# Kernel tuning notes

Hardware: AMD Instinct MI355X
Metric: run time of the kernel (lower is better)

The kernel has to match this reference:

```python
import jax, jax.numpy as jnp
import numpy as np

TEMP = 0.05
EPS = 1e-8  # torch CosineSimilarity default eps


def _normalize(x):
    # torch cosine_similarity clamps norm at eps
    n = jnp.maximum(jnp.linalg.norm(x, axis=-1, keepdims=True), EPS)
    return x / n


def setup_inputs() -> dict:
    key = jax.random.key(0)
    k1, k2, k3 = jax.random.split(key, 3)
    N, D = 4096, 1024
    return {
        "repr_sent": jax.random.normal(k1, (N, D), dtype=jnp.float32),
        "repr_pos": jax.random.normal(k2, (N, D), dtype=jnp.float32),
        "repr_neg": jax.random.normal(k3, (N, D), dtype=jnp.float32),
    }


def reference(repr_sent, repr_pos, repr_neg):
    # Normalize then GEMM instead of broadcasting an [N, 2N, D] intermediate.
    s = _normalize(repr_sent)            # [N, D]
    p = _normalize(repr_pos)             # [N, D]
    n = _normalize(repr_neg)             # [N, D]
    cand = jnp.concatenate([p, n], axis=0)           # [2N, D]
    sim = jnp.einsum("nd,md->nm", s, cand) / TEMP    # [N, 2N]
    # Cross-entropy with labels = arange(N) (positive is the i-th column)
    logz = jax.nn.logsumexp(sim, axis=-1)            # [N]
    N_ = sim.shape[0]
    pos_logit = jnp.diagonal(sim[:, :N_])            # sim[i, i]
    loss = jnp.mean(logz - pos_logit)
    return loss
```

## Files before the change

kernel.cpp:

```cpp
#include <hip/hip_runtime.h>
#include <stdint.h>

#define N_ROWS 4096
#define D_DIM  1024
#define N_CAND 8192
#define TEMP_INV 20.0f
#define QSCALE 508.0f
#define OUT_SCALE (TEMP_INV / (QSCALE * QSCALE))

#define BM 256
#define BN 256
#define BK 64
#define NT 16

typedef __attribute__((ext_vector_type(4))) int   i32x4;

using gvoid = __attribute__((address_space(1))) void;
using lvoid = __attribute__((address_space(3))) void;

#define BAR() __builtin_amdgcn_s_barrier()
#define SCHED0() __builtin_amdgcn_sched_barrier(0)

__global__ __launch_bounds__(256) void prep_kernel(
    const float* __restrict__ s, const float* __restrict__ p,
    const float* __restrict__ ng, unsigned char* __restrict__ s_q,
    unsigned char* __restrict__ cand_q, float* __restrict__ rowsum) {
  const int row = blockIdx.x;
  const int t = threadIdx.x;
  const float* src;
  unsigned char* dst;
  if (row < N_ROWS) {
    src = s + (size_t)row * D_DIM;
    dst = s_q + (size_t)row * D_DIM;
  } else if (row < 2 * N_ROWS) {
    src = p + (size_t)(row - N_ROWS) * D_DIM;
    dst = cand_q + (size_t)(row - N_ROWS) * D_DIM;
  } else {
    src = ng + (size_t)(row - 2 * N_ROWS) * D_DIM;
    dst = cand_q + (size_t)(row - N_ROWS) * D_DIM;
  }

  float4 v = reinterpret_cast<const float4*>(src)[t];
  float ss = v.x * v.x + v.y * v.y + v.z * v.z + v.w * v.w;
#pragma unroll
  for (int m = 32; m >= 1; m >>= 1) ss += __shfl_xor(ss, m, 64);
  __shared__ float red[4];
  const int w = t >> 6, l = t & 63;
  if (l == 0) red[w] = ss;
  __syncthreads();
  const float tot = red[0] + red[1] + red[2] + red[3];
  const float qs = QSCALE / fmaxf(sqrtf(tot), 1e-8f);

  auto q8 = [&](float x) -> unsigned {
    return (unsigned)((int)rintf(fminf(fmaxf(x * qs, -127.0f), 127.0f))) &
           0xffu;
  };
  const unsigned pk =
      q8(v.x) | (q8(v.y) << 8) | (q8(v.z) << 16) | (q8(v.w) << 24);
  *reinterpret_cast<unsigned*>(dst + t * 4) = pk;

  if (t == 0 && row < N_ROWS) rowsum[row] = 0.0f;
}

__global__ __launch_bounds__(512) void gemm_lse_kernel(
    const unsigned char* __restrict__ s_q,
    const unsigned char* __restrict__ cand_q,
    float* __restrict__ rowsum, float* __restrict__ pos) {
  __shared__ __align__(16) unsigned char lds[4 * 32768];

  const int t = threadIdx.x;
  const int w = t >> 6;
  const int l = t & 63;
  const int g = l >> 4;
  const int rl = l & 15;
  const int wm = w >> 2;
  const int wn = w & 3;
  const int slot = (g + (rl >> 1)) & 3;
  const int rowBase = blockIdx.y * BM;
  const int colBase = blockIdx.x * BN;

  i32x4 acc[8][4] = {};
  i32x4 af[8];
  i32x4 bf[4];

  const int sRow = t >> 2;
  const int sSlotL = ((t & 3) - (t >> 3)) & 3;
  const unsigned char* gA =
      s_q + (size_t)(rowBase + sRow) * D_DIM + sSlotL * 16;
  const unsigned char* gB =
      cand_q + (size_t)(colBase + sRow) * D_DIM + sSlotL * 16;

  auto stage = [&](int T) {
    const int buf = (T & 3) * 32768;
    const size_t ko = (size_t)T * 64;
#pragma unroll
    for (int h = 0; h < 2; ++h) {
      __builtin_amdgcn_global_load_lds(
          (const gvoid*)(gA + ko + (size_t)h * (128 * D_DIM)),
          (lvoid*)(lds + buf + h * 8192 + t * 16), 16, 0, 0);
      __builtin_amdgcn_global_load_lds(
          (const gvoid*)(gB + ko + (size_t)h * (128 * D_DIM)),
          (lvoid*)(lds + buf + 16384 + h * 8192 + t * 16), 16, 0, 0);
    }
  };

  stage(0); stage(1);
  asm volatile("s_waitcnt vmcnt(4)" ::: "memory");
  SCHED0();
  BAR(); SCHED0();

  for (int T = 0; T < NT; ++T) {
    const unsigned char* A = lds + (T & 3) * 32768;
    const unsigned char* B = A + 16384;
#pragma unroll
    for (int m = 0; m < 8; ++m) {
      const int r = wm * 128 + m * 16 + rl;
      af[m] = *reinterpret_cast<const i32x4*>(A + r * 64 + slot * 16);
    }
#pragma unroll
    for (int n = 0; n < 4; ++n) {
      const int r = wn * 64 + n * 16 + rl;
      bf[n] = *reinterpret_cast<const i32x4*>(B + r * 64 + slot * 16);
    }
    if (T + 2 < NT) stage(T + 2);

    __builtin_amdgcn_s_setprio(1);
#pragma unroll
    for (int m = 0; m < 8; ++m)
#pragma unroll
      for (int n = 0; n < 4; ++n)
        acc[m][n] = __builtin_amdgcn_mfma_i32_16x16x64_i8(
            af[m], bf[n], acc[m][n], 0, 0, 0);
    __builtin_amdgcn_s_setprio(0);

    if (T <= NT - 3) {
      asm volatile("s_waitcnt vmcnt(4)" ::: "memory");
    } else if (T == NT - 2) {
      asm volatile("s_waitcnt vmcnt(0)" ::: "memory");
    }
    SCHED0();
    BAR(); SCHED0();
  }

  __syncthreads();
  float* red = reinterpret_cast<float*>(lds);
  if (t < BM) red[t] = 0.0f;
  __syncthreads();

#pragma unroll
  for (int m = 0; m < 8; ++m) {
#pragma unroll
    for (int j = 0; j < 4; ++j) {
      const int rloc = wm * 128 + m * 16 + g * 4 + j;
      const int rowg = rowBase + rloc;
      float sm = 0.0f;
#pragma unroll
      for (int n = 0; n < 4; ++n) {
        const int colg = colBase + wn * 64 + n * 16 + rl;
        const float simv = (float)acc[m][n][j] * OUT_SCALE;
        if (colg == rowg) pos[rowg] = simv;
        sm += __expf(simv - TEMP_INV);
      }
      sm += __shfl_xor(sm, 1, 64);
      sm += __shfl_xor(sm, 2, 64);
      sm += __shfl_xor(sm, 4, 64);
      sm += __shfl_xor(sm, 8, 64);
      if (rl == 0) atomicAdd(&red[rloc], sm);
    }
  }
  __syncthreads();
  if (t < BM) atomicAdd(&rowsum[rowBase + t], red[t]);
}

__global__ __launch_bounds__(1024) void loss_kernel(
    const float* __restrict__ rowsum, const float* __restrict__ pos,
    float* __restrict__ out) {
  const int t = threadIdx.x;
  float acc = 0.0f;
  for (int i = t; i < N_ROWS; i += 1024)
    acc += TEMP_INV + logf(rowsum[i]) - pos[i];
#pragma unroll
  for (int m = 32; m >= 1; m >>= 1) acc += __shfl_xor(acc, m, 64);
  __shared__ float red[16];
  const int w = t >> 6, l = t & 63;
  if (l == 0) red[w] = acc;
  __syncthreads();
  if (t == 0) {
    float tot = 0.0f;
#pragma unroll
    for (int i = 0; i < 16; ++i) tot += red[i];
    out[0] = tot / (float)N_ROWS;
  }
}

extern "C" void kernel_launch(void* const* d_in, const int* in_sizes, int n_in,
                              void* d_out, int out_size, void* d_ws,
                              size_t ws_size, hipStream_t stream) {
  (void)in_sizes; (void)n_in; (void)out_size; (void)ws_size;
  const float* s = (const float*)d_in[0];
  const float* p = (const float*)d_in[1];
  const float* ng = (const float*)d_in[2];

  unsigned char* s_q = (unsigned char*)d_ws;
  unsigned char* cand_q = s_q + (size_t)N_ROWS * D_DIM;
  float* rowsum = (float*)(cand_q + (size_t)N_CAND * D_DIM);
  float* pos = rowsum + N_ROWS;
  float* out = (float*)d_out;

  prep_kernel<<<dim3(3 * N_ROWS), dim3(256), 0, stream>>>(s, p, ng, s_q,
                                                          cand_q, rowsum);
  gemm_lse_kernel<<<dim3(N_CAND / BN, N_ROWS / BM), dim3(512), 0, stream>>>(
      s_q, cand_q, rowsum, pos);
  loss_kernel<<<dim3(1), dim3(1024), 0, stream>>>(rowsum, pos, out);
}
```

Before: 64.42 us.

## Load A fragments directly from global memory and stage only B through LDS

```diff
diff --git a/kernel.cpp b/kernel.cpp
--- a/kernel.cpp
+++ b/kernel.cpp
@@ -13,7 +13,7 @@
 #define BK 64
 #define NT 16
 
-typedef __attribute__((ext_vector_type(4))) int   i32x4;
+typedef __attribute__((ext_vector_type(4))) int i32x4;
 
 using gvoid = __attribute__((address_space(1))) void;
 using lvoid = __attribute__((address_space(3))) void;
@@ -66,76 +66,72 @@
     const unsigned char* __restrict__ s_q,
     const unsigned char* __restrict__ cand_q,
     float* __restrict__ rowsum, float* __restrict__ pos) {
-  __shared__ __align__(16) unsigned char lds[4 * 32768];
+  __shared__ __align__(16) unsigned char lds[4 * 16384];
 
   const int t = threadIdx.x;
   const int w = t >> 6;
   const int l = t & 63;
   const int g = l >> 4;
   const int rl = l & 15;
-  const int wm = w >> 2;
-  const int wn = w & 3;
+  const int wm = w >> 1;
+  const int wn = w & 1;
   const int slot = (g + (rl >> 1)) & 3;
   const int rowBase = blockIdx.y * BM;
   const int colBase = blockIdx.x * BN;
 
-  i32x4 acc[8][4] = {};
-  i32x4 af[8];
-  i32x4 bf[4];
+  i32x4 acc[4][8] = {};
+  i32x4 af[4];
+  i32x4 bf[8];
+
+  const unsigned char* gAf =
+      s_q + (size_t)(rowBase + wm * 64 + rl) * D_DIM + g * 16;
 
   const int sRow = t >> 2;
   const int sSlotL = ((t & 3) - (t >> 3)) & 3;
-  const unsigned char* gA =
-      s_q + (size_t)(rowBase + sRow) * D_DIM + sSlotL * 16;
   const unsigned char* gB =
       cand_q + (size_t)(colBase + sRow) * D_DIM + sSlotL * 16;
 
-  auto stage = [&](int T) {
-    const int buf = (T & 3) * 32768;
+  auto stageB = [&](int T) {
+    const int buf = (T & 3) * 16384;
     const size_t ko = (size_t)T * 64;
-#pragma unroll
-    for (int h = 0; h < 2; ++h) {
-      __builtin_amdgcn_global_load_lds(
-          (const gvoid*)(gA + ko + (size_t)h * (128 * D_DIM)),
-          (lvoid*)(lds + buf + h * 8192 + t * 16), 16, 0, 0);
-      __builtin_amdgcn_global_load_lds(
-          (const gvoid*)(gB + ko + (size_t)h * (128 * D_DIM)),
-          (lvoid*)(lds + buf + 16384 + h * 8192 + t * 16), 16, 0, 0);
-    }
+    __builtin_amdgcn_global_load_lds((const gvoid*)(gB + ko),
+                                     (lvoid*)(lds + buf + t * 16), 16, 0, 0);
+    __builtin_amdgcn_global_load_lds(
+        (const gvoid*)(gB + ko + (size_t)128 * D_DIM),
+        (lvoid*)(lds + buf + 8192 + t * 16), 16, 0, 0);
   };
 
-  stage(0); stage(1);
-  asm volatile("s_waitcnt vmcnt(4)" ::: "memory");
+  stageB(0); stageB(1);
+  asm volatile("s_waitcnt vmcnt(2)" ::: "memory");
   SCHED0();
   BAR(); SCHED0();
 
   for (int T = 0; T < NT; ++T) {
-    const unsigned char* A = lds + (T & 3) * 32768;
-    const unsigned char* B = A + 16384;
-#pragma unroll
-    for (int m = 0; m < 8; ++m) {
-      const int r = wm * 128 + m * 16 + rl;
-      af[m] = *reinterpret_cast<const i32x4*>(A + r * 64 + slot * 16);
-    }
-#pragma unroll
-    for (int n = 0; n < 4; ++n) {
-      const int r = wn * 64 + n * 16 + rl;
+#pragma unroll
+    for (int m = 0; m < 4; ++m)
+      af[m] = *reinterpret_cast<const i32x4*>(
+          gAf + (size_t)m * (16 * D_DIM) + T * 64);
+    if (T + 2 < NT) stageB(T + 2);
+
+    const unsigned char* B = lds + (T & 3) * 16384;
+#pragma unroll
+    for (int n = 0; n < 8; ++n) {
+      const int r = wn * 128 + n * 16 + rl;
       bf[n] = *reinterpret_cast<const i32x4*>(B + r * 64 + slot * 16);
     }
-    if (T + 2 < NT) stage(T + 2);
 
     __builtin_amdgcn_s_setprio(1);
 #pragma unroll
-    for (int m = 0; m < 8; ++m)
-#pragma unroll
-      for (int n = 0; n < 4; ++n)
+    for (int m = 0; m < 4; ++m)
+#pragma unroll
+      for (int n = 0; n < 8; ++n)
         acc[m][n] = __builtin_amdgcn_mfma_i32_16x16x64_i8(
             af[m], bf[n], acc[m][n], 0, 0, 0);
     __builtin_amdgcn_s_setprio(0);
 
-    if (T <= NT - 3) {
-      asm volatile("s_waitcnt vmcnt(4)" ::: "memory");
-    } else if (T == NT - 2) {
+    if (T + 2 < NT) {
+      asm volatile("s_waitcnt vmcnt(2)" ::: "memory");
+    } else {
       asm volatile("s_waitcnt vmcnt(0)" ::: "memory");
     }
     SCHED0();
@@ -148,15 +144,15 @@
   __syncthreads();
 
 #pragma unroll
-  for (int m = 0; m < 8; ++m) {
+  for (int m = 0; m < 4; ++m) {
 #pragma unroll
     for (int j = 0; j < 4; ++j) {
-      const int rloc = wm * 128 + m * 16 + g * 4 + j;
+      const int rloc = wm * 64 + m * 16 + g * 4 + j;
       const int rowg = rowBase + rloc;
       float sm = 0.0f;
 #pragma unroll
-      for (int n = 0; n < 4; ++n) {
-        const int colg = colBase + wn * 64 + n * 16 + rl;
+      for (int n = 0; n < 8; ++n) {
+        const int colg = colBase + wn * 128 + n * 16 + rl;
         const float simv = (float)acc[m][n][j] * OUT_SCALE;
         if (colg == rowg) pos[rowg] = simv;
         sm += __expf(simv - TEMP_INV);
```

Result: slower. 76.04 us (+18.0%).

## Split each K-step into two half-tile phases interleaving LDS reads, loads and MFMAs

Applied to the files above, without the earlier changes.

```diff
diff --git a/kernel.cpp b/kernel.cpp
--- a/kernel.cpp
+++ b/kernel.cpp
@@ -13,13 +13,15 @@
 #define BK 64
 #define NT 16
 
-typedef __attribute__((ext_vector_type(4))) int   i32x4;
+typedef __attribute__((ext_vector_type(4))) int i32x4;
 
 using gvoid = __attribute__((address_space(1))) void;
 using lvoid = __attribute__((address_space(3))) void;
 
 #define BAR() __builtin_amdgcn_s_barrier()
 #define SCHED0() __builtin_amdgcn_sched_barrier(0)
+#define LGKM0() do { asm volatile("s_waitcnt lgkmcnt(0)" ::: "memory"); \
+                     __builtin_amdgcn_sched_barrier(0); } while (0)
 
 __global__ __launch_bounds__(256) void prep_kernel(
     const float* __restrict__ s, const float* __restrict__ p,
@@ -80,7 +82,7 @@
   const int colBase = blockIdx.x * BN;
 
   i32x4 acc[8][4] = {};
-  i32x4 af[8];
+  i32x4 af[4];
   i32x4 bf[4];
 
   const int sRow = t >> 2;
@@ -90,21 +92,26 @@
   const unsigned char* gB =
       cand_q + (size_t)(colBase + sRow) * D_DIM + sSlotL * 16;
 
-  auto stage = [&](int T) {
+  auto stageA = [&](int T) {
     const int buf = (T & 3) * 32768;
     const size_t ko = (size_t)T * 64;
 #pragma unroll
-    for (int h = 0; h < 2; ++h) {
+    for (int h = 0; h < 2; ++h)
       __builtin_amdgcn_global_load_lds(
           (const gvoid*)(gA + ko + (size_t)h * (128 * D_DIM)),
           (lvoid*)(lds + buf + h * 8192 + t * 16), 16, 0, 0);
+  };
+  auto stageB = [&](int T) {
+    const int buf = (T & 3) * 32768;
+    const size_t ko = (size_t)T * 64;
+#pragma unroll
+    for (int h = 0; h < 2; ++h)
       __builtin_amdgcn_global_load_lds(
           (const gvoid*)(gB + ko + (size_t)h * (128 * D_DIM)),
           (lvoid*)(lds + buf + 16384 + h * 8192 + t * 16), 16, 0, 0);
-    }
   };
 
-  stage(0); stage(1);
+  stageA(0); stageB(0); stageA(1); stageB(1);
   asm volatile("s_waitcnt vmcnt(4)" ::: "memory");
   SCHED0();
   BAR(); SCHED0();
@@ -112,28 +119,47 @@
   for (int T = 0; T < NT; ++T) {
     const unsigned char* A = lds + (T & 3) * 32768;
     const unsigned char* B = A + 16384;
-#pragma unroll
-    for (int m = 0; m < 8; ++m) {
-      const int r = wm * 128 + m * 16 + rl;
-      af[m] = *reinterpret_cast<const i32x4*>(A + r * 64 + slot * 16);
-    }
+    const bool sN = (T + 2 < NT);
+
 #pragma unroll
     for (int n = 0; n < 4; ++n) {
       const int r = wn * 64 + n * 16 + rl;
       bf[n] = *reinterpret_cast<const i32x4*>(B + r * 64 + slot * 16);
     }
-    if (T + 2 < NT) stage(T + 2);
-
+#pragma unroll
+    for (int m = 0; m < 4; ++m) {
+      const int r = wm * 128 + m * 16 + rl;
+      af[m] = *reinterpret_cast<const i32x4*>(A + r * 64 + slot * 16);
+    }
+    if (sN) stageA(T + 2);
+    BAR(); LGKM0();
     __builtin_amdgcn_s_setprio(1);
 #pragma unroll
-    for (int m = 0; m < 8; ++m)
+    for (int m = 0; m < 4; ++m)
 #pragma unroll
       for (int n = 0; n < 4; ++n)
         acc[m][n] = __builtin_amdgcn_mfma_i32_16x16x64_i8(
             af[m], bf[n], acc[m][n], 0, 0, 0);
     __builtin_amdgcn_s_setprio(0);
-
-    if (T <= NT - 3) {
+    BAR();
+
+#pragma unroll
+    for (int m = 0; m < 4; ++m) {
+      const int r = wm * 128 + (m + 4) * 16 + rl;
+      af[m] = *reinterpret_cast<const i32x4*>(A + r * 64 + slot * 16);
+    }
+    if (sN) stageB(T + 2);
+    BAR(); LGKM0();
+    __builtin_amdgcn_s_setprio(1);
+#pragma unroll
+    for (int m = 0; m < 4; ++m)
+#pragma unroll
+      for (int n = 0; n < 4; ++n)
+        acc[m + 4][n] = __builtin_amdgcn_mfma_i32_16x16x64_i8(
+            af[m], bf[n], acc[m + 4][n], 0, 0, 0);
+    __builtin_amdgcn_s_setprio(0);
+
+    if (sN) {
       asm volatile("s_waitcnt vmcnt(4)" ::: "memory");
     } else if (T == NT - 2) {
       asm volatile("s_waitcnt vmcnt(0)" ::: "memory");
```

Result: no change. 64.30 us (-0.2%).
